# Kernel optimization log

Measured on AMD Instinct MI355X. Metric: run time of the kernel, lower is better.

Reference implementation:

```python
import jax, jax.numpy as jnp
import numpy as np
from jax import lax

NH, KD, HD = 8, 16, 32        # num_heads, key_dim, head_dim
SCALE = KD ** -0.5            # 0.25


def _conv(x, w, b, groups=1):
    # x: (B,C,H,W), w: (O, C//groups, kh, kw), 'SAME' padding, stride 1
    y = lax.conv_general_dilated(
        x, w, window_strides=(1, 1), padding='SAME',
        dimension_numbers=('NCHW', 'OIHW', 'NCHW'),
        feature_group_count=groups)
    return y + b[None, :, None, None]


def setup_inputs() -> dict:
    key = jax.random.key(0)
    k0, k1, k2, k3 = jax.random.split(key, 4)
    B, C, H, W = 4, 256, 48, 48
    qkv_c = NH * (4 * KD + HD)  # 768
    return {
        'x': jax.random.normal(k0, (B, C, H, W), jnp.float32),
        'rcv_w': jax.random.normal(k1, (qkv_c, C, 1, 1), jnp.float32) * 0.05,
        'rcv_b': jnp.zeros((qkv_c,), jnp.float32),
        'pe_w': jax.random.normal(k2, (C, 1, 3, 3), jnp.float32) * 0.05,
        'pe_b': jnp.zeros((C,), jnp.float32),
        'proj_w': jax.random.normal(k3, (C, C, 1, 1), jnp.float32) * 0.05,
        'proj_b': jnp.zeros((C,), jnp.float32),
    }


def reference(x, rcv_w, rcv_b, pe_w, pe_b, proj_w, proj_b):
    B, C, H, W = x.shape
    # fused row/col q,k and v projection (1x1 conv)
    rcv = _conv(x, rcv_w, rcv_b).reshape(B, NH, 4 * KD + HD, H, W)
    rq, rk, cq, ck, v = jnp.split(rcv, [KD, 2 * KD, 3 * KD, 4 * KD], axis=2)
    # row attention over height: (B,nh,H,H,W), softmax over first H axis
    attn_r = jnp.einsum('bndiw,bndjw->bnijw', rq, rk) * SCALE
    # column attention over width: (B,nh,W,H,W), softmax over first W axis
    attn_w = jnp.einsum('bndhi,bndhj->bnihj', cq, ck) * SCALE
    attn_r = jax.nn.softmax(attn_r, axis=2)
    attn_w = jax.nn.softmax(attn_w, axis=2)
    # sandwiched value contraction: contract row index i, then col index j
    t = jnp.einsum('bnihw,bndij->bndjhw', attn_r, v)   # (B,nh,d,W,H,W)
    out = jnp.einsum('bndjhw,bnjhw->bndhw', t, attn_w).reshape(B, C, H, W)
    # conv positional encoding on v (depthwise 3x3) + output projection
    out = out + _conv(v.reshape(B, C, H, W), pe_w, pe_b, groups=C)
    return _conv(out, proj_w, proj_b)
```

## Files before the change

kernel.cpp:

```cpp
#include <hip/hip_runtime.h>

#define S_ 2304

typedef unsigned short u16;
typedef unsigned int u32;
typedef __attribute__((ext_vector_type(8))) short bf16x8;
typedef __attribute__((ext_vector_type(4))) float f32x4;

static __device__ __forceinline__ u16 f2bf(float x) {
  union { float f; unsigned u; } v; v.f = x;
  unsigned r = v.u + 0x7FFFu + ((v.u >> 16) & 1u);
  return (u16)(r >> 16);
}
static __device__ __forceinline__ float bf2f(u16 h) {
  union { unsigned u; float f; } v; v.u = ((unsigned)h) << 16; return v.f;
}
static __device__ __forceinline__ float bflo(unsigned p) {
  union { unsigned u; float f; } v; v.u = p << 16; return v.f;
}
static __device__ __forceinline__ float bfhi(unsigned p) {
  union { unsigned u; float f; } v; v.u = p & 0xFFFF0000u; return v.f;
}

__global__ __launch_bounds__(256) void prep_kernel(
    const float* __restrict__ w0, u16* __restrict__ wh0, u16* __restrict__ wl0,
    const float* __restrict__ w1, u16* __restrict__ wh1, u16* __restrict__ wl1,
    const float* __restrict__ x, u16* __restrict__ xTh)
{
  __shared__ u16 tile[64][65];
  const int bid = blockIdx.x;
  const int tid = threadIdx.x;
  if (bid < 256) {
    const float* w; u16 *wh, *wl; int id;
    if (bid < 192) { w = w0; wh = wh0; wl = wl0; id = bid * 256 + tid; }
    else { w = w1; wh = wh1; wl = wl1; id = (bid - 192) * 256 + tid; }
    float4 v = ((const float4*)w)[id];
    short4 h, l;
    float f[4] = {v.x, v.y, v.z, v.w};
    u16 hh[4], ll[4];
#pragma unroll
    for (int q = 0; q < 4; q++) {
      hh[q] = f2bf(f[q]);
      ll[q] = f2bf(f[q] - bf2f(hh[q]));
    }
    h.x = hh[0]; h.y = hh[1]; h.z = hh[2]; h.w = hh[3];
    l.x = ll[0]; l.y = ll[1]; l.z = ll[2]; l.w = ll[3];
    ((short4*)wh)[id] = h;
    ((short4*)wl)[id] = l;
    return;
  }
  const int bid2 = bid - 256;
  const int s0 = (bid2 % 36) * 64, c0 = ((bid2 / 36) % 4) * 64, b = bid2 / 144;
  const float* inb = x + (size_t)b * 256 * S_;
  u16* oh = xTh + (size_t)b * S_ * 256;
#pragma unroll
  for (int it = 0; it < 4; it++) {
    int id = tid + it * 256;
    int c = id >> 4, s4 = (id & 15) * 4;
    float4 v = *(const float4*)&inb[(size_t)(c0 + c) * S_ + s0 + s4];
    tile[s4 + 0][c] = f2bf(v.x);
    tile[s4 + 1][c] = f2bf(v.y);
    tile[s4 + 2][c] = f2bf(v.z);
    tile[s4 + 3][c] = f2bf(v.w);
  }
  __syncthreads();
#pragma unroll
  for (int it = 0; it < 4; it++) {
    int id = tid + it * 256;
    int s = id >> 4, c4 = (id & 15) * 4;
    short4 h;
    h.x = (short)tile[s][c4 + 0]; h.y = (short)tile[s][c4 + 1];
    h.z = (short)tile[s][c4 + 2]; h.w = (short)tile[s][c4 + 3];
    *(short4*)&oh[(size_t)(s0 + s) * 256 + c0 + c4] = h;
  }
}

__global__ __launch_bounds__(256) void split_transpose_kernel(
    const float* __restrict__ in, u16* __restrict__ outh, u16* __restrict__ outl)
{
  __shared__ unsigned tile[64][65];
  const int s0 = blockIdx.x * 64, c0 = blockIdx.y * 64, b = blockIdx.z;
  const float* inb = in + (size_t)b * 256 * S_;
  u16* oh = outh + (size_t)b * S_ * 256;
  u16* ol = outl + (size_t)b * S_ * 256;
  const int tid = threadIdx.x;
#pragma unroll
  for (int it = 0; it < 4; it++) {
    int id = tid + it * 256;
    int c = id >> 4, s4 = (id & 15) * 4;
    float4 v = *(const float4*)&inb[(size_t)(c0 + c) * S_ + s0 + s4];
    float f[4] = {v.x, v.y, v.z, v.w};
#pragma unroll
    for (int q = 0; q < 4; q++) {
      u16 h = f2bf(f[q]);
      u16 l = f2bf(f[q] - bf2f(h));
      tile[s4 + q][c] = (unsigned)h | ((unsigned)l << 16);
    }
  }
  __syncthreads();
#pragma unroll
  for (int it = 0; it < 4; it++) {
    int id = tid + it * 256;
    int s = id >> 4, c4 = (id & 15) * 4;
    short4 h, l;
    unsigned p0 = tile[s][c4 + 0], p1 = tile[s][c4 + 1];
    unsigned p2 = tile[s][c4 + 2], p3 = tile[s][c4 + 3];
    h.x = (short)(p0 & 0xffff); h.y = (short)(p1 & 0xffff);
    h.z = (short)(p2 & 0xffff); h.w = (short)(p3 & 0xffff);
    l.x = (short)(p0 >> 16); l.y = (short)(p1 >> 16);
    l.z = (short)(p2 >> 16); l.w = (short)(p3 >> 16);
    *(short4*)&oh[(size_t)(s0 + s) * 256 + c0 + c4] = h;
    *(short4*)&ol[(size_t)(s0 + s) * 256 + c0 + c4] = l;
  }
}

__global__ __launch_bounds__(256) void gemm_mfma_kernel(
    const u16* __restrict__ Wh, const u16* __restrict__ Wl,
    const float* __restrict__ bias,
    const u16* __restrict__ XTh, u32* __restrict__ qkvP)
{
  __shared__ u16 wAh[2][64 * 40];
  __shared__ u16 wAl[2][64 * 40];
  const int MB = 12;
  const int xcd = blockIdx.x & 7;
  const int idx = blockIdx.x >> 3;
  const int g = xcd * 9 + idx / MB;
  const int mb = idx % MB;
  const int nb = g % 18, b = g / 18;
  const int m0 = mb * 64, n0 = nb * 128;
  const int tid = threadIdx.x;
  const int wv = tid >> 6, lane = tid & 63;
  const int lr = lane & 15, lg = lane >> 4;
  const bf16x8 zv = {0, 0, 0, 0, 0, 0, 0, 0};

  const u16* xbh = XTh + ((size_t)b * S_ + n0 + wv * 32) * 256;

  f32x4 acc[4][2];
#pragma unroll
  for (int mt = 0; mt < 4; mt++)
#pragma unroll
    for (int nt = 0; nt < 2; nt++) acc[mt][nt] = (f32x4){0.f, 0.f, 0.f, 0.f};

#define STAGE_W(t, buf)                                                      \
  {                                                                          \
    _Pragma("unroll")                                                        \
    for (int r = 0; r < 2; r++) {                                            \
      int id = tid + r * 256;                                                \
      int m = id >> 3, k4 = (id & 7) * 4;                                    \
      *(short4*)&wAh[buf][m * 40 + k4] =                                     \
          *(const short4*)&Wh[(size_t)(m0 + m) * 256 + (t) * 32 + k4];       \
      *(short4*)&wAl[buf][m * 40 + k4] =                                     \
          *(const short4*)&Wl[(size_t)(m0 + m) * 256 + (t) * 32 + k4];       \
    }                                                                        \
  }

  STAGE_W(0, 0);
  bf16x8 cbh[2];
#pragma unroll
  for (int nt = 0; nt < 2; nt++) {
    size_t off = (size_t)(nt * 16 + lr) * 256 + lg * 8;
    cbh[nt] = *(const bf16x8*)&xbh[off];
  }
  __syncthreads();

  for (int t = 0; t < 8; t++) {
    int buf = t & 1;
    if (t < 7) STAGE_W(t + 1, buf ^ 1);

    bf16x8 nbh[2];
    if (t < 7) {
#pragma unroll
      for (int nt = 0; nt < 2; nt++) {
        size_t off = (size_t)(nt * 16 + lr) * 256 + (t + 1) * 32 + lg * 8;
        nbh[nt] = *(const bf16x8*)&xbh[off];
      }
    } else {
#pragma unroll
      for (int nt = 0; nt < 2; nt++) nbh[nt] = zv;
    }

    bf16x8 ah[4], al[4];
#pragma unroll
    for (int mt = 0; mt < 4; mt++) {
      ah[mt] = *(const bf16x8*)&wAh[buf][(mt * 16 + lr) * 40 + lg * 8];
      al[mt] = *(const bf16x8*)&wAl[buf][(mt * 16 + lr) * 40 + lg * 8];
    }
#pragma unroll
    for (int mt = 0; mt < 4; mt++)
#pragma unroll
      for (int nt = 0; nt < 2; nt++) {
        acc[mt][nt] = __builtin_amdgcn_mfma_f32_16x16x32_bf16(ah[mt], cbh[nt], acc[mt][nt], 0, 0, 0);
        acc[mt][nt] = __builtin_amdgcn_mfma_f32_16x16x32_bf16(al[mt], cbh[nt], acc[mt][nt], 0, 0, 0);
      }
    __syncthreads();
#pragma unroll
    for (int nt = 0; nt < 2; nt++) cbh[nt] = nbh[nt];
  }

#pragma unroll
  for (int mt = 0; mt < 4; mt++) {
    int mb_ = m0 + mt * 16 + lg * 4;
    float4 b4 = *(const float4*)&bias[mb_];
    int head = mb_ / 96, pl = mb_ % 96;
    size_t rowoff = ((size_t)(b * 8 + head) * 48 + (pl >> 1)) * S_;
#pragma unroll
    for (int nt = 0; nt < 2; nt++) {
      int s = n0 + wv * 32 + nt * 16 + lr;
      u16 h0 = f2bf(acc[mt][nt][0] + b4.x);
      u16 h1 = f2bf(acc[mt][nt][1] + b4.y);
      u16 h2 = f2bf(acc[mt][nt][2] + b4.z);
      u16 h3 = f2bf(acc[mt][nt][3] + b4.w);
      qkvP[rowoff + s]      = (u32)h0 | ((u32)h1 << 16);
      qkvP[rowoff + S_ + s] = (u32)h2 | ((u32)h3 << 16);
    }
  }
#undef STAGE_W
}

__global__ __launch_bounds__(256) void gemm_n64_kernel(
    const u16* __restrict__ Wh, const u16* __restrict__ Wl,
    const float* __restrict__ bias,
    const u16* __restrict__ XTh, const u16* __restrict__ XTl,
    float* __restrict__ Out)
{
  __shared__ u16 wAh[2][64 * 40];
  __shared__ u16 wAl[2][64 * 40];
  const int M = 256, MB = 4;
  const int xcd = blockIdx.x & 7;
  const int idx = blockIdx.x >> 3;
  const int g = xcd * 18 + idx / MB;
  const int mb = idx % MB;
  const int nb = g % 36, b = g / 36;
  const int m0 = mb * 64, n0 = nb * 64;
  const int tid = threadIdx.x;
  const int wv = tid >> 6, lane = tid & 63;
  const int wm = wv >> 1, wsd = wv & 1;
  const int lr = lane & 15, lg = lane >> 4;
  const bf16x8 zv = {0, 0, 0, 0, 0, 0, 0, 0};

  const u16* xbh = XTh + ((size_t)b * S_ + n0 + wsd * 32) * 256;
  const u16* xbl = XTl + ((size_t)b * S_ + n0 + wsd * 32) * 256;

  f32x4 acc[2][2];
#pragma unroll
  for (int mt = 0; mt < 2; mt++)
#pragma unroll
    for (int nt = 0; nt < 2; nt++) acc[mt][nt] = (f32x4){0.f, 0.f, 0.f, 0.f};

#define STAGE_W(t, buf)                                                      \
  {                                                                          \
    _Pragma("unroll")                                                        \
    for (int r = 0; r < 2; r++) {                                            \
      int id = tid + r * 256;                                                \
      int m = id >> 3, k4 = (id & 7) * 4;                                    \
      *(short4*)&wAh[buf][m * 40 + k4] =                                     \
          *(const short4*)&Wh[(size_t)(m0 + m) * 256 + (t) * 32 + k4];       \
      *(short4*)&wAl[buf][m * 40 + k4] =                                     \
          *(const short4*)&Wl[(size_t)(m0 + m) * 256 + (t) * 32 + k4];       \
    }                                                                        \
  }

  STAGE_W(0, 0);
  bf16x8 cbh[2], cbl[2];
#pragma unroll
  for (int nt = 0; nt < 2; nt++) {
    size_t off = (size_t)(nt * 16 + lr) * 256 + lg * 8;
    cbh[nt] = *(const bf16x8*)&xbh[off];
    cbl[nt] = *(const bf16x8*)&xbl[off];
  }
  __syncthreads();

  for (int t = 0; t < 8; t++) {
    int buf = t & 1;
    if (t < 7) STAGE_W(t + 1, buf ^ 1);

    bf16x8 nbh[2], nbl[2];
    if (t < 7) {
#pragma unroll
      for (int nt = 0; nt < 2; nt++) {
        size_t off = (size_t)(nt * 16 + lr) * 256 + (t + 1) * 32 + lg * 8;
        nbh[nt] = *(const bf16x8*)&xbh[off];
        nbl[nt] = *(const bf16x8*)&xbl[off];
      }
    } else {
#pragma unroll
      for (int nt = 0; nt < 2; nt++) { nbh[nt] = zv; nbl[nt] = zv; }
    }

    bf16x8 ah[2], al[2];
#pragma unroll
    for (int mt = 0; mt < 2; mt++) {
      ah[mt] = *(const bf16x8*)&wAh[buf][(wm * 32 + mt * 16 + lr) * 40 + lg * 8];
      al[mt] = *(const bf16x8*)&wAl[buf][(wm * 32 + mt * 16 + lr) * 40 + lg * 8];
    }
#pragma unroll
    for (int mt = 0; mt < 2; mt++)
#pragma unroll
      for (int nt = 0; nt < 2; nt++) {
        acc[mt][nt] = __builtin_amdgcn_mfma_f32_16x16x32_bf16(ah[mt], cbh[nt], acc[mt][nt], 0, 0, 0);
        acc[mt][nt] = __builtin_amdgcn_mfma_f32_16x16x32_bf16(ah[mt], cbl[nt], acc[mt][nt], 0, 0, 0);
        acc[mt][nt] = __builtin_amdgcn_mfma_f32_16x16x32_bf16(al[mt], cbh[nt], acc[mt][nt], 0, 0, 0);
      }
    __syncthreads();
#pragma unroll
    for (int nt = 0; nt < 2; nt++) { cbh[nt] = nbh[nt]; cbl[nt] = nbl[nt]; }
  }

  float* ob = Out + (size_t)b * M * S_;
#pragma unroll
  for (int mt = 0; mt < 2; mt++) {
    float4 b4 = *(const float4*)&bias[m0 + wm * 32 + mt * 16 + lg * 4];
    float bv[4] = {b4.x, b4.y, b4.z, b4.w};
#pragma unroll
    for (int nt = 0; nt < 2; nt++) {
      int s = n0 + wsd * 32 + nt * 16 + lr;
#pragma unroll
      for (int r = 0; r < 4; r++) {
        int m = m0 + wm * 32 + mt * 16 + lg * 4 + r;
        ob[(size_t)m * S_ + s] = acc[mt][nt][r] + bv[r];
      }
    }
  }
#undef STAGE_W
}

__global__ __launch_bounds__(256) void scores_kernel(
    const u32* __restrict__ qkv, u16* __restrict__ arF, u16* __restrict__ awF)
{
  __shared__ float Sm[2][48 * 49];
  __shared__ float red1[2][48];
  __shared__ u32 rkp[2][8 * 48];
  __shared__ u32 cqp[2][8 * 48], ckp[2][8 * 48];
  const int bid = blockIdx.x;
  const int tid = threadIdx.x;

  if (bid < 512) {
    const int hg = bid & 15, n = (bid >> 4) & 7, b = bid >> 7;
    const u32* base = qkv + (size_t)(b * 8 + n) * 48 * S_;
    u32 rqp[9][8];
#pragma unroll
    for (int k = 0; k < 9; k++) {
      int p = tid + k * 256;
#pragma unroll
      for (int d8 = 0; d8 < 8; d8++)
        rqp[k][d8] = base[(size_t)d8 * S_ + p];
    }
    {
      int h = hg * 3;
      for (int id = tid; id < 384; id += 256)
        rkp[0][id] = base[(size_t)(8 + id / 48) * S_ + h * 48 + (id % 48)];
    }
    __syncthreads();
    for (int hh = 0; hh < 3; hh++) {
      const int buf = hh & 1;
      const int h = hg * 3 + hh;
#pragma unroll
      for (int k = 0; k < 9; k++) {
        int p = tid + k * 256;
        int i = p / 48, w = p % 48;
        float s = 0.f;
#pragma unroll
        for (int d8 = 0; d8 < 8; d8++) {
          u32 a = rqp[k][d8], c = rkp[buf][d8 * 48 + w];
          s += bflo(a) * bflo(c) + bfhi(a) * bfhi(c);
        }
        Sm[buf][i * 49 + w] = s * 0.25f;
      }
      if (hh < 2) {
        int hn = h + 1;
        for (int id = tid; id < 384; id += 256)
          rkp[buf ^ 1][id] = base[(size_t)(8 + id / 48) * S_ + hn * 48 + (id % 48)];
      }
      __syncthreads();
      if (tid < 192) {
        int w = tid >> 2, e = tid & 3;
        float m = -1e30f;
        for (int i = e; i < 48; i += 4) m = fmaxf(m, Sm[buf][i * 49 + w]);
        m = fmaxf(m, __shfl_xor(m, 1));
        m = fmaxf(m, __shfl_xor(m, 2));
        float s = 0.f;
        for (int i = e; i < 48; i += 4) {
          float ev = __expf(Sm[buf][i * 49 + w] - m);
          Sm[buf][i * 49 + w] = ev;
          s += ev;
        }
        s += __shfl_xor(s, 1);
        s += __shfl_xor(s, 2);
        red1[buf][w] = 1.0f / s;
      }
      __syncthreads();
      u16* dst = arF + ((size_t)(b * 8 + n) * 48 + h) * 2304;
      for (int id = tid; id < 576; id += 256) {
        int nt = id / 192, rem = id % 192, mt = rem / 64, l = rem % 64;
        int w = nt * 16 + (l & 15);
        int i0 = mt * 16 + ((l >> 4) << 2);
        float rs = red1[buf][w];
        short4 o;
        o.x = (short)f2bf(Sm[buf][(i0 + 0) * 49 + w] * rs);
        o.y = (short)f2bf(Sm[buf][(i0 + 1) * 49 + w] * rs);
        o.z = (short)f2bf(Sm[buf][(i0 + 2) * 49 + w] * rs);
        o.w = (short)f2bf(Sm[buf][(i0 + 3) * 49 + w] * rs);
        *(short4*)&dst[id * 4] = o;
      }
    }
  } else {
    const int bid2 = bid - 512;
    const int hg = bid2 & 15, n = (bid2 >> 4) & 7, b = bid2 >> 7;
    const u32* base = qkv + (size_t)(b * 8 + n) * 48 * S_;
    {
      int h = hg * 3;
      for (int id = tid; id < 384; id += 256) {
        cqp[0][id] = base[(size_t)(16 + id / 48) * S_ + h * 48 + (id % 48)];
        ckp[0][id] = base[(size_t)(24 + id / 48) * S_ + h * 48 + (id % 48)];
      }
    }
    __syncthreads();
    for (int hh = 0; hh < 3; hh++) {
      const int buf = hh & 1;
      const int h = hg * 3 + hh;
      for (int id = tid; id < 2304; id += 256) {
        int w = id / 48, j = id % 48;
        float t = 0.f;
#pragma unroll
        for (int d8 = 0; d8 < 8; d8++) {
          u32 c = ckp[buf][d8 * 48 + w], a = cqp[buf][d8 * 48 + j];
          t += bflo(c) * bflo(a) + bfhi(c) * bfhi(a);
        }
        Sm[buf][w * 49 + j] = t * 0.25f;
      }
      if (hh < 2) {
        int hn = h + 1;
        for (int id = tid; id < 384; id += 256) {
          cqp[buf ^ 1][id] = base[(size_t)(16 + id / 48) * S_ + hn * 48 + (id % 48)];
          ckp[buf ^ 1][id] = base[(size_t)(24 + id / 48) * S_ + hn * 48 + (id % 48)];
        }
      }
      __syncthreads();
      if (tid < 192) {
        int w = tid >> 2, e = tid & 3;
        float m = -1e30f;
        for (int j = e; j < 48; j += 4) m = fmaxf(m, Sm[buf][w * 49 + j]);
        m = fmaxf(m, __shfl_xor(m, 1));
        m = fmaxf(m, __shfl_xor(m, 2));
        float s = 0.f;
        for (int j = e; j < 48; j += 4) {
          float ev = __expf(Sm[buf][w * 49 + j] - m);
          Sm[buf][w * 49 + j] = ev;
          s += ev;
        }
        s += __shfl_xor(s, 1);
        s += __shfl_xor(s, 2);
        red1[buf][w] = 1.0f / s;
      }
      __syncthreads();
      u16* dst = awF + ((size_t)(b * 8 + n) * 48 + h) * 3072;
      for (int id = tid; id < 384; id += 256) {
        int nt = id / 128, rem = id % 128, ks = rem / 64, l = rem % 64;
        int w = nt * 16 + (l & 15);
        int j0 = ks * 32 + ((l >> 4) << 3);
        float rs = red1[buf][w];
        u16 t8[8];
#pragma unroll
        for (int e = 0; e < 8; e++) {
          int j = j0 + e;
          t8[e] = (j < 48) ? f2bf(Sm[buf][w * 49 + j] * rs) : (u16)0;
        }
        short4 o0, o1;
        o0.x = (short)t8[0]; o0.y = (short)t8[1]; o0.z = (short)t8[2]; o0.w = (short)t8[3];
        o1.x = (short)t8[4]; o1.y = (short)t8[5]; o1.z = (short)t8[6]; o1.w = (short)t8[7];
        *(short4*)&dst[id * 8]     = o0;
        *(short4*)&dst[id * 8 + 4] = o1;
      }
    }
  }
}

__global__ __launch_bounds__(256) void attn_main_kernel(
    const u32* __restrict__ qkv, const u16* __restrict__ arF,
    const u16* __restrict__ awF, const float* __restrict__ pe_w,
    const float* __restrict__ pe_b, float* __restrict__ y)
{
  __shared__ u16 vA[96 * 72];
  const int id0 = blockIdx.x;
  const int n = id0 & 7;
  const int rest = id0 >> 3;
  const int b = rest >> 6;
  const int inner = rest & 63;
  const int dchunk = inner >> 2;
  const int hc = inner & 3;
  const int tid = threadIdx.x;
  const int wave = tid >> 6, lane = tid & 63;
  const int dl = wave >> 1, half = wave & 1;
  const int h0 = hc * 12 + half * 6;
  const int lr = lane & 15, lg = lane >> 4;

  for (int id = tid; id < 96 * 24; id += 256) {
    int row = id / 24, col = 48 + id % 24;
    vA[row * 72 + col] = 0;
  }
  const u32* vrow = qkv + ((size_t)(b * 8 + n) * 48 + 32 + dchunk) * S_;
  for (int id = tid; id < 576; id += 256) {
    int i = id / 12, j4 = (id % 12) * 4;
    uint4 v = *(const uint4*)&vrow[i * 48 + j4];
    short4 lo, hi;
    lo.x = (short)(v.x & 0xffff); hi.x = (short)(v.x >> 16);
    lo.y = (short)(v.y & 0xffff); hi.y = (short)(v.y >> 16);
    lo.z = (short)(v.z & 0xffff); hi.z = (short)(v.z >> 16);
    lo.w = (short)(v.w & 0xffff); hi.w = (short)(v.w >> 16);
    *(short4*)&vA[i * 72 + j4] = lo;
    *(short4*)&vA[(48 + i) * 72 + j4] = hi;
  }
  __syncthreads();

  const size_t bn48 = (size_t)(b * 8 + n) * 48;
  const int c = n * 32 + dchunk * 2 + dl;
  float pw[9];
#pragma unroll
  for (int t = 0; t < 9; t++) pw[t] = pe_w[c * 9 + t];
  const float pb = pe_b[c];
  float* yg = y + ((size_t)b * 256 + c) * S_;
  const int vrow0 = dl * 48;

  for (int hh = 0; hh < 6; hh++) {
    int h = h0 + hh;
    const u16* awg = awF + (bn48 + h) * 3072;
    const u16* arg = arF + (bn48 + h) * 2304;

    bf16x8 bf0[3], bf1[3];
#pragma unroll
    for (int nt = 0; nt < 3; nt++) {
      bf0[nt] = *(const bf16x8*)&awg[nt * 1024 + lane * 8];
      bf1[nt] = *(const bf16x8*)&awg[nt * 1024 + 512 + lane * 8];
    }

    f32x4 acc[3][3];
#pragma unroll
    for (int mt = 0; mt < 3; mt++)
#pragma unroll
      for (int nt = 0; nt < 3; nt++) acc[mt][nt] = (f32x4){0.f, 0.f, 0.f, 0.f};

#pragma unroll
    for (int mt = 0; mt < 3; mt++) {
      bf16x8 a0 = *(const bf16x8*)&vA[(vrow0 + mt * 16 + lr) * 72 + lg * 8];
      bf16x8 a1 = *(const bf16x8*)&vA[(vrow0 + mt * 16 + lr) * 72 + 32 + lg * 8];
#pragma unroll
      for (int nt = 0; nt < 3; nt++) {
        acc[mt][nt] = __builtin_amdgcn_mfma_f32_16x16x32_bf16(a0, bf0[nt], acc[mt][nt], 0, 0, 0);
        acc[mt][nt] = __builtin_amdgcn_mfma_f32_16x16x32_bf16(a1, bf1[nt], acc[mt][nt], 0, 0, 0);
      }
    }

    float pv[3];
#pragma unroll
    for (int nt = 0; nt < 3; nt++) {
      float p = 0.f;
#pragma unroll
      for (int mt = 0; mt < 3; mt++) {
        short4 s = *(const short4*)&arg[(nt * 3 + mt) * 256 + lane * 4];
        p += bf2f((u16)s.x) * acc[mt][nt][0] + bf2f((u16)s.y) * acc[mt][nt][1]
           + bf2f((u16)s.z) * acc[mt][nt][2] + bf2f((u16)s.w) * acc[mt][nt][3];
      }
      p += __shfl_xor(p, 16);
      p += __shfl_xor(p, 32);
      pv[nt] = p;
    }

    if (lane < 48) {
      float a = (lane < 16) ? pv[0] : (lane < 32 ? pv[1] : pv[2]);
      a += pb;
      int ww = lane;
#pragma unroll
      for (int kh = -1; kh <= 1; kh++) {
        int ih = h + kh;
        if (ih < 0 || ih > 47) continue;
#pragma unroll
        for (int kw = -1; kw <= 1; kw++) {
          int jw = ww + kw;
          if (jw < 0 || jw > 47) continue;
          a += pw[(kh + 1) * 3 + (kw + 1)] * bf2f(vA[(vrow0 + ih) * 72 + jw]);
        }
      }
      yg[h * 48 + ww] = a;
    }
  }
}

extern "C" void kernel_launch(void* const* d_in, const int* in_sizes, int n_in,
                              void* d_out, int out_size, void* d_ws, size_t ws_size,
                              hipStream_t stream) {
  const float* x      = (const float*)d_in[0];
  const float* rcv_w  = (const float*)d_in[1];
  const float* rcv_b  = (const float*)d_in[2];
  const float* pe_w   = (const float*)d_in[3];
  const float* pe_b   = (const float*)d_in[4];
  const float* proj_w = (const float*)d_in[5];
  const float* proj_b = (const float*)d_in[6];
  float* out = (float*)d_out;

  char* ws = (char*)d_ws;
  u32*   qkvP = (u32*)ws;
  u16*   arF = (u16*)(ws + 14155776);
  u16*   awF = (u16*)(ws + 21233664);
  u16*   xTh = (u16*)(ws + 30670848);
  float* y   = (float*)(ws + 35389440);
  u16*   Whr = (u16*)(ws + 44826624);
  u16*   Wlr = (u16*)(ws + 45219840);
  u16*   Whp = (u16*)(ws + 45613056);
  u16*   Wlp = (u16*)(ws + 45744128);
  u16*   yTh = arF;
  u16*   yTl = awF;

  prep_kernel<<<dim3(832), 256, 0, stream>>>(rcv_w, Whr, Wlr, proj_w, Whp, Wlp, x, xTh);
  gemm_mfma_kernel<<<dim3(72 * 12), 256, 0, stream>>>(Whr, Wlr, rcv_b, xTh, qkvP);
  scores_kernel<<<dim3(1024), 256, 0, stream>>>(qkvP, arF, awF);
  attn_main_kernel<<<dim3(2048), 256, 0, stream>>>(qkvP, arF, awF, pe_w, pe_b, y);
  split_transpose_kernel<<<dim3(36, 4, 4), 256, 0, stream>>>(y, yTh, yTl);
  gemm_n64_kernel<<<dim3(576), 256, 0, stream>>>(Whp, Wlp, proj_b, yTh, yTl, out);
}
```

Baseline: 113.1 us.

## Fuse bf16 hi/lo split into attention epilogue and drop split-transpose kernel

The attention kernel now writes its output as packed bf16 hi/lo pairs in channel-major layout, and the projection GEMM reads this packed layout directly with strided per-element loads, unpacking in registers. This removes the separate split_transpose kernel launch and its extra round trip of the fp32 intermediate through memory. In exchange, the GEMM's B-operand loads become 16 scalar strided 32-bit loads per tile instead of vectorised contiguous loads, which may hurt load efficiency.

```diff
diff --git a/kernel.cpp b/kernel.cpp
--- a/kernel.cpp
+++ b/kernel.cpp
@@ -72,45 +72,6 @@
     h.x = (short)tile[s][c4 + 0]; h.y = (short)tile[s][c4 + 1];
     h.z = (short)tile[s][c4 + 2]; h.w = (short)tile[s][c4 + 3];
     *(short4*)&oh[(size_t)(s0 + s) * 256 + c0 + c4] = h;
-  }
-}
-
-__global__ __launch_bounds__(256) void split_transpose_kernel(
-    const float* __restrict__ in, u16* __restrict__ outh, u16* __restrict__ outl)
-{
-  __shared__ unsigned tile[64][65];
-  const int s0 = blockIdx.x * 64, c0 = blockIdx.y * 64, b = blockIdx.z;
-  const float* inb = in + (size_t)b * 256 * S_;
-  u16* oh = outh + (size_t)b * S_ * 256;
-  u16* ol = outl + (size_t)b * S_ * 256;
-  const int tid = threadIdx.x;
-#pragma unroll
-  for (int it = 0; it < 4; it++) {
-    int id = tid + it * 256;
-    int c = id >> 4, s4 = (id & 15) * 4;
-    float4 v = *(const float4*)&inb[(size_t)(c0 + c) * S_ + s0 + s4];
-    float f[4] = {v.x, v.y, v.z, v.w};
-#pragma unroll
-    for (int q = 0; q < 4; q++) {
-      u16 h = f2bf(f[q]);
-      u16 l = f2bf(f[q] - bf2f(h));
-      tile[s4 + q][c] = (unsigned)h | ((unsigned)l << 16);
-    }
-  }
-  __syncthreads();
-#pragma unroll
-  for (int it = 0; it < 4; it++) {
-    int id = tid + it * 256;
-    int s = id >> 4, c4 = (id & 15) * 4;
-    short4 h, l;
-    unsigned p0 = tile[s][c4 + 0], p1 = tile[s][c4 + 1];
-    unsigned p2 = tile[s][c4 + 2], p3 = tile[s][c4 + 3];
-    h.x = (short)(p0 & 0xffff); h.y = (short)(p1 & 0xffff);
-    h.z = (short)(p2 & 0xffff); h.w = (short)(p3 & 0xffff);
-    l.x = (short)(p0 >> 16); l.y = (short)(p1 >> 16);
-    l.z = (short)(p2 >> 16); l.w = (short)(p3 >> 16);
-    *(short4*)&oh[(size_t)(s0 + s) * 256 + c0 + c4] = h;
-    *(short4*)&ol[(size_t)(s0 + s) * 256 + c0 + c4] = l;
   }
 }
 
@@ -220,8 +181,7 @@
 __global__ __launch_bounds__(256) void gemm_n64_kernel(
     const u16* __restrict__ Wh, const u16* __restrict__ Wl,
     const float* __restrict__ bias,
-    const u16* __restrict__ XTh, const u16* __restrict__ XTl,
-    float* __restrict__ Out)
+    const u32* __restrict__ yP, float* __restrict__ Out)
 {
   __shared__ u16 wAh[2][64 * 40];
   __shared__ u16 wAl[2][64 * 40];
@@ -236,10 +196,9 @@
   const int wv = tid >> 6, lane = tid & 63;
   const int wm = wv >> 1, wsd = wv & 1;
   const int lr = lane & 15, lg = lane >> 4;
-  const bf16x8 zv = {0, 0, 0, 0, 0, 0, 0, 0};
-
-  const u16* xbh = XTh + ((size_t)b * S_ + n0 + wsd * 32) * 256;
-  const u16* xbl = XTl + ((size_t)b * S_ + n0 + wsd * 32) * 256;
+
+  const u32* yb = yP + (size_t)b * 256 * S_;
+  const int s0 = n0 + wsd * 32;
 
   f32x4 acc[2][2];
 #pragma unroll
@@ -260,31 +219,34 @@
     }                                                                        \
   }
 
+#define LOAD_B(t, dst)                                                       \
+  {                                                                          \
+    _Pragma("unroll")                                                        \
+    for (int nt = 0; nt < 2; nt++) {                                         \
+      int s = s0 + nt * 16 + lr;                                             \
+      _Pragma("unroll")                                                      \
+      for (int e = 0; e < 8; e++)                                            \
+        dst[nt][e] = yb[(size_t)((t) * 32 + lg * 8 + e) * S_ + s];           \
+    }                                                                        \
+  }
+
   STAGE_W(0, 0);
-  bf16x8 cbh[2], cbl[2];
-#pragma unroll
-  for (int nt = 0; nt < 2; nt++) {
-    size_t off = (size_t)(nt * 16 + lr) * 256 + lg * 8;
-    cbh[nt] = *(const bf16x8*)&xbh[off];
-    cbl[nt] = *(const bf16x8*)&xbl[off];
-  }
+  u32 cb[2][8];
+  LOAD_B(0, cb);
   __syncthreads();
 
   for (int t = 0; t < 8; t++) {
     int buf = t & 1;
     if (t < 7) STAGE_W(t + 1, buf ^ 1);
 
-    bf16x8 nbh[2], nbl[2];
+    u32 nbv[2][8];
     if (t < 7) {
-#pragma unroll
-      for (int nt = 0; nt < 2; nt++) {
-        size_t off = (size_t)(nt * 16 + lr) * 256 + (t + 1) * 32 + lg * 8;
-        nbh[nt] = *(const bf16x8*)&xbh[off];
-        nbl[nt] = *(const bf16x8*)&xbl[off];
-      }
+      LOAD_B(t + 1, nbv);
     } else {
 #pragma unroll
-      for (int nt = 0; nt < 2; nt++) { nbh[nt] = zv; nbl[nt] = zv; }
+      for (int nt = 0; nt < 2; nt++)
+#pragma unroll
+        for (int e = 0; e < 8; e++) nbv[nt][e] = 0;
     }
 
     bf16x8 ah[2], al[2];
@@ -293,17 +255,27 @@
       ah[mt] = *(const bf16x8*)&wAh[buf][(wm * 32 + mt * 16 + lr) * 40 + lg * 8];
       al[mt] = *(const bf16x8*)&wAl[buf][(wm * 32 + mt * 16 + lr) * 40 + lg * 8];
     }
+    bf16x8 bh[2], bl[2];
+#pragma unroll
+    for (int nt = 0; nt < 2; nt++)
+#pragma unroll
+      for (int e = 0; e < 8; e++) {
+        bh[nt][e] = (short)(cb[nt][e] & 0xffffu);
+        bl[nt][e] = (short)(cb[nt][e] >> 16);
+      }
 #pragma unroll
     for (int mt = 0; mt < 2; mt++)
 #pragma unroll
       for (int nt = 0; nt < 2; nt++) {
-        acc[mt][nt] = __builtin_amdgcn_mfma_f32_16x16x32_bf16(ah[mt], cbh[nt], acc[mt][nt], 0, 0, 0);
-        acc[mt][nt] = __builtin_amdgcn_mfma_f32_16x16x32_bf16(ah[mt], cbl[nt], acc[mt][nt], 0, 0, 0);
-        acc[mt][nt] = __builtin_amdgcn_mfma_f32_16x16x32_bf16(al[mt], cbh[nt], acc[mt][nt], 0, 0, 0);
+        acc[mt][nt] = __builtin_amdgcn_mfma_f32_16x16x32_bf16(ah[mt], bh[nt], acc[mt][nt], 0, 0, 0);
+        acc[mt][nt] = __builtin_amdgcn_mfma_f32_16x16x32_bf16(ah[mt], bl[nt], acc[mt][nt], 0, 0, 0);
+        acc[mt][nt] = __builtin_amdgcn_mfma_f32_16x16x32_bf16(al[mt], bh[nt], acc[mt][nt], 0, 0, 0);
       }
     __syncthreads();
 #pragma unroll
-    for (int nt = 0; nt < 2; nt++) { cbh[nt] = nbh[nt]; cbl[nt] = nbl[nt]; }
+    for (int nt = 0; nt < 2; nt++)
+#pragma unroll
+      for (int e = 0; e < 8; e++) cb[nt][e] = nbv[nt][e];
   }
 
   float* ob = Out + (size_t)b * M * S_;
@@ -322,6 +294,7 @@
     }
   }
 #undef STAGE_W
+#undef LOAD_B
 }
 
 __global__ __launch_bounds__(256) void scores_kernel(
@@ -478,7 +451,7 @@
 __global__ __launch_bounds__(256) void attn_main_kernel(
     const u32* __restrict__ qkv, const u16* __restrict__ arF,
     const u16* __restrict__ awF, const float* __restrict__ pe_w,
-    const float* __restrict__ pe_b, float* __restrict__ y)
+    const float* __restrict__ pe_b, u32* __restrict__ yP)
 {
   __shared__ u16 vA[96 * 72];
   const int id0 = blockIdx.x;
@@ -518,7 +491,7 @@
 #pragma unroll
   for (int t = 0; t < 9; t++) pw[t] = pe_w[c * 9 + t];
   const float pb = pe_b[c];
-  float* yg = y + ((size_t)b * 256 + c) * S_;
+  u32* yg = yP + ((size_t)b * 256 + c) * S_;
   const int vrow0 = dl * 48;
 
   for (int hh = 0; hh < 6; hh++) {
@@ -580,7 +553,9 @@
           a += pw[(kh + 1) * 3 + (kw + 1)] * bf2f(vA[(vrow0 + ih) * 72 + jw]);
         }
       }
-      yg[h * 48 + ww] = a;
+      u16 hh16 = f2bf(a);
+      u16 ll16 = f2bf(a - bf2f(hh16));
+      yg[h * 48 + ww] = (u32)hh16 | ((u32)ll16 << 16);
     }
   }
 }
@@ -602,18 +577,15 @@
   u16*   arF = (u16*)(ws + 14155776);
   u16*   awF = (u16*)(ws + 21233664);
   u16*   xTh = (u16*)(ws + 30670848);
-  float* y   = (float*)(ws + 35389440);
+  u32*   yP  = (u32*)(ws + 35389440);
   u16*   Whr = (u16*)(ws + 44826624);
   u16*   Wlr = (u16*)(ws + 45219840);
   u16*   Whp = (u16*)(ws + 45613056);
   u16*   Wlp = (u16*)(ws + 45744128);
-  u16*   yTh = arF;
-  u16*   yTl = awF;
 
   prep_kernel<<<dim3(832), 256, 0, stream>>>(rcv_w, Whr, Wlr, proj_w, Whp, Wlp, x, xTh);
   gemm_mfma_kernel<<<dim3(72 * 12), 256, 0, stream>>>(Whr, Wlr, rcv_b, xTh, qkvP);
   scores_kernel<<<dim3(1024), 256, 0, stream>>>(qkvP, arF, awF);
-  attn_main_kernel<<<dim3(2048), 256, 0, stream>>>(qkvP, arF, awF, pe_w, pe_b, y);
-  split_transpose_kernel<<<dim3(36, 4, 4), 256, 0, stream>>>(y, yTh, yTl);
-  gemm_n64_kernel<<<dim3(576), 256, 0, stream>>>(Whp, Wlp, proj_b, yTh, yTl, out);
-}
+  attn_main_kernel<<<dim3(2048), 256, 0, stream>>>(qkvP, arF, awF, pe_w, pe_b, yP);
+  gemm_n64_kernel<<<dim3(576), 256, 0, stream>>>(Whp, Wlp, proj_b, yP, out);
+}
```

Result: faster. 98.87 us (-12.6%).
